# Kernel tuning notes

Hardware: AMD Instinct MI355X
Metric: run time of the kernel (lower is better)

Reference implementation:

```python
import jax, jax.numpy as jnp
import numpy as np

NUM_HEADS = 16
THETA = 10000.0


def apply_rope(x, pos, theta):
    # x: [B, H, S, d], pos: [S] int
    d = x.shape[-1]
    inv_freq = theta ** (-jnp.arange(0, d, 2, dtype=jnp.float32) / d)  # [d/2]
    ang = pos.astype(jnp.float32)[:, None] * inv_freq  # [S, d/2]
    cos, sin = jnp.cos(ang), jnp.sin(ang)
    x1, x2 = x[..., 0::2], x[..., 1::2]
    out_even = x1 * cos - x2 * sin
    out_odd = x1 * sin + x2 * cos
    return jnp.stack([out_even, out_odd], axis=-1).reshape(x.shape)


def setup_inputs() -> dict:
    key = jax.random.key(0)
    ks = jax.random.split(key, 5)
    B, S, D = 4, 2048, 2048
    s = 1.0 / np.sqrt(D)
    return {
        "x": jax.random.normal(ks[0], (B, S, D), dtype=jnp.float32),
        "token_positions": jnp.arange(S, dtype=jnp.int32),
        "wq": jax.random.normal(ks[1], (D, D), dtype=jnp.float32) * s,
        "wk": jax.random.normal(ks[2], (D, D), dtype=jnp.float32) * s,
        "wv": jax.random.normal(ks[3], (D, D), dtype=jnp.float32) * s,
        "wo": jax.random.normal(ks[4], (D, D), dtype=jnp.float32) * s,
    }


def reference(x, token_positions, wq, wk, wv, wo):
    B, S, _ = x.shape
    H = NUM_HEADS
    dh = wq.shape[0] // H

    def proj(w):
        y = jnp.einsum('bsd,ed->bse', x, w)  # Linear: x @ W^T
        return y.reshape(B, S, H, dh).transpose(0, 2, 1, 3)  # [B,H,S,dh]

    Q, K, V = proj(wq), proj(wk), proj(wv)
    Q = apply_rope(Q, token_positions, THETA)
    K = apply_rope(K, token_positions, THETA)

    scores = jnp.einsum('bhqd,bhkd->bhqk', Q, K) / jnp.sqrt(jnp.float32(dh))
    causal = jnp.tril(jnp.ones((S, S), dtype=bool))
    scores = jnp.where(causal, scores, jnp.finfo(scores.dtype).min)
    attn = jax.nn.softmax(scores, axis=-1)
    out = jnp.einsum('bhqk,bhkd->bhqd', attn, V)
    out = out.transpose(0, 2, 1, 3).reshape(B, S, H * dh)
    return jnp.einsum('bsd,ed->bse', out, wo)
```

## Files before the change

### kernel.cpp

```cpp
#include <hip/hip_runtime.h>
#include <math.h>

typedef __bf16 bf16;
typedef bf16 bf16x8 __attribute__((ext_vector_type(8)));
typedef bf16 bf16x4v __attribute__((ext_vector_type(4)));
typedef float f32x4 __attribute__((ext_vector_type(4)));

#define BB 4
#define SS 2048
#define DD 2048
#define HH 16
#define DH 128

__device__ __forceinline__ void gload_lds16(const bf16* g, bf16* l) {
  __builtin_amdgcn_global_load_lds(
      (const __attribute__((address_space(1))) void*)g,
      (__attribute__((address_space(3))) void*)l, 16, 0, 0);
}

__global__ __launch_bounds__(256) void cast_kernel(const float* __restrict__ in,
                                                   bf16* __restrict__ out, int n4) {
  int i = blockIdx.x * blockDim.x + threadIdx.x;
  if (i < n4) {
    const float4 v = ((const float4*)in)[i];
    bf16x4v o = {(bf16)v.x, (bf16)v.y, (bf16)v.z, (bf16)v.w};
    ((bf16x4v*)out)[i] = o;
  }
}

__global__ __launch_bounds__(256) void cast4_kernel(const float* __restrict__ w0,
                                                    const float* __restrict__ w1,
                                                    const float* __restrict__ w2,
                                                    const float* __restrict__ w3,
                                                    bf16* __restrict__ out) {
  const int i = blockIdx.x * blockDim.x + threadIdx.x;
  const int per = (DD * DD) / 4;
  const int sel = i / per, off = i - sel * per;
  const float* src = (sel == 0) ? w0 : (sel == 1) ? w1 : (sel == 2) ? w2 : w3;
  const float4 v = ((const float4*)src)[off];
  bf16x4v o = {(bf16)v.x, (bf16)v.y, (bf16)v.z, (bf16)v.w};
  ((bf16x4v*)(out + (size_t)sel * DD * DD))[off] = o;
}

template <int MODE>
__global__ __launch_bounds__(256) void gemm_bt(const bf16* __restrict__ A,
                                               const bf16* __restrict__ Bw,
                                               bf16* __restrict__ Cb,
                                               float* __restrict__ Cf,
                                               const int* __restrict__ pos,
                                               int M, int N, int K) {
  __shared__ alignas(16) bf16 lA[128 * 64];
  __shared__ alignas(16) bf16 lB[128 * 64];
  const int tid = threadIdx.x;
  const int wave = tid >> 6, lane = tid & 63;
  const int quad = lane >> 4, l15 = lane & 15;
  const int m0 = blockIdx.y * 128, n0 = blockIdx.x * 128;
  const int wm = (wave >> 1) * 64, wn = (wave & 1) * 64;

  f32x4 acc[4][4] = {};

  for (int k0 = 0; k0 < K; k0 += 64) {
    __syncthreads();
#pragma unroll
    for (int i = 0; i < 4; ++i) {
      const int p = (wave * 4 + i) * 64 + lane;
      const int r = p >> 3, c = p & 7;
      gload_lds16(A + (size_t)(m0 + r) * K + k0 + c * 8, lA + (size_t)(wave * 4 + i) * 512);
      gload_lds16(Bw + (size_t)(n0 + r) * K + k0 + c * 8, lB + (size_t)(wave * 4 + i) * 512);
    }
    __syncthreads();
#pragma unroll
    for (int kk = 0; kk < 2; ++kk) {
      bf16x8 af[4], bfr[4];
#pragma unroll
      for (int t = 0; t < 4; ++t)
        af[t] = *(const bf16x8*)(lA + (wm + t * 16 + l15) * 64 + kk * 32 + quad * 8);
#pragma unroll
      for (int t = 0; t < 4; ++t)
        bfr[t] = *(const bf16x8*)(lB + (wn + t * 16 + l15) * 64 + kk * 32 + quad * 8);
#pragma unroll
      for (int mt = 0; mt < 4; ++mt)
#pragma unroll
        for (int nt = 0; nt < 4; ++nt)
          acc[mt][nt] = __builtin_amdgcn_mfma_f32_16x16x32_bf16(af[mt], bfr[nt], acc[mt][nt], 0, 0, 0);
    }
  }

  float ps[4][4];
  if (MODE == 0) {
#pragma unroll
    for (int mt = 0; mt < 4; ++mt)
#pragma unroll
      for (int r = 0; r < 4; ++r)
        ps[mt][r] = (float)pos[(m0 + wm + mt * 16 + quad * 4 + r) & (SS - 1)];
  }

#pragma unroll
  for (int nt = 0; nt < 4; ++nt) {
    const int col = n0 + wn + nt * 16 + l15;
    float invf = 0.f, sgn = 0.f;
    if (MODE == 0) {
      const int d = col & (DH - 1);
      invf = exp2f((float)(d >> 1) * (-13.28771238f / 64.0f));
      sgn = (d & 1) ? 1.0f : -1.0f;
    }
#pragma unroll
    for (int mt = 0; mt < 4; ++mt) {
#pragma unroll
      for (int r = 0; r < 4; ++r) {
        const int row = m0 + wm + mt * 16 + quad * 4 + r;
        float v = acc[mt][nt][r];
        if (MODE == 0) {
          const float partner = __shfl_xor(v, 1);
          float sn, cn;
          __sincosf(ps[mt][r] * invf, &sn, &cn);
          v = fmaf(partner, sgn * sn, v * cn);
          const int b = row >> 11, s = row & (SS - 1);
          const int h = col >> 7, d = col & (DH - 1);
          Cb[((((size_t)b * HH + h) * SS + s) << 7) + d] = (bf16)v;
        } else if (MODE == 1) {
          const int b = row >> 11, s = row & (SS - 1);
          const int h = col >> 7, d = col & (DH - 1);
          Cb[(((size_t)b * HH + h) * DH + d) * SS + s] = (bf16)v;
        } else {
          Cf[(size_t)row * N + col] = v;
        }
      }
    }
  }
}

__global__ __launch_bounds__(256, 2) void flash_attn(const bf16* __restrict__ Q,
                                                     const bf16* __restrict__ Kg,
                                                     const bf16* __restrict__ Vt,
                                                     bf16* __restrict__ O) {
  __shared__ alignas(16) bf16 lK[2][64 * 128];
  __shared__ alignas(16) bf16 lV[2][128 * 64];
  __shared__ alignas(16) bf16 lP[4][16 * 64];

  const int tid = threadIdx.x;
  const int wave = tid >> 6, lane = tid & 63;
  const int quad = lane >> 4, l15 = lane & 15;
  const int swz = l15 & 7;
  const int bh = blockIdx.y;
  const int q0 = (gridDim.x - 1 - blockIdx.x) * 64;
  const bf16* Qh = Q + (size_t)bh * SS * DH;
  const bf16* Kh = Kg + (size_t)bh * SS * DH;
  const bf16* Vh = Vt + (size_t)bh * DH * SS;
  const int nkb = (q0 >> 6) + 1;

  bf16x8 qf[4];
#pragma unroll
  for (int t = 0; t < 4; ++t)
    qf[t] = *(const bf16x8*)(Qh + (size_t)(q0 + wave * 16 + l15) * DH + t * 32 + quad * 8);

  bf16* lPw = &lP[wave][0];
  const float cs = 0.12751649736f;
  const float MSTAT = 20.0f;
  float lsum = 0.f;
  f32x4 oacc[8] = {};

  auto stage = [&](bf16* kbuf, bf16* vbuf, int kb) {
#pragma unroll
    for (int j = 0; j < 4; ++j) {
      const int c = tid + j * 256;
      const int cb = wave * 64 + j * 256;
      const int kr = c >> 4;
      gload_lds16(Kh + (size_t)(kb * 64 + kr) * DH + (((c & 15) ^ (kr & 7)) * 8),
                  kbuf + (size_t)cb * 8);
      const int vr = c >> 3;
      gload_lds16(Vh + (size_t)vr * SS + kb * 64 + (((c & 7) ^ (vr & 7)) * 8),
                  vbuf + (size_t)cb * 8);
    }
  };

  int cur = 0;

  auto kv_iter = [&](bool diagf) {
    const bf16* kcur = lK[cur];
    const bf16* vcur = lV[cur];
    const int ktlim = diagf ? wave : 3;

    f32x4 sacc[4];
#pragma unroll
    for (int kt = 0; kt < 4; ++kt) sacc[kt] = (f32x4){0.f, 0.f, 0.f, 0.f};
    __builtin_amdgcn_s_setprio(1);
#pragma unroll
    for (int kt = 0; kt < 4; ++kt) {
      if (kt <= ktlim) {
#pragma unroll
        for (int t = 0; t < 4; ++t) {
          const bf16x8 kfrag =
              *(const bf16x8*)(kcur + (kt * 16 + l15) * 128 + (((t * 4 + quad) ^ swz) * 8));
          sacc[kt] = __builtin_amdgcn_mfma_f32_16x16x32_bf16(kfrag, qf[t], sacc[kt], 0, 0, 0);
        }
      }
    }
    __builtin_amdgcn_s_setprio(0);

#pragma unroll
    for (int kt = 0; kt < 4; ++kt) {
      bf16x4v pk = {(bf16)0.f, (bf16)0.f, (bf16)0.f, (bf16)0.f};
      if (kt <= ktlim) {
        float ls = 0.f;
#pragma unroll
        for (int r = 0; r < 4; ++r) {
          float e = exp2f(fmaf(sacc[kt][r], cs, -MSTAT));
          if (diagf && kt == wave && (quad * 4 + r) > l15) e = 0.f;
          ls += e;
          pk[r] = (bf16)e;
        }
        lsum += ls;
      }
      *(bf16x4v*)(lPw + l15 * 64 + (((kt * 2 + (quad >> 1)) ^ swz) * 8) + (quad & 1) * 4) = pk;
    }

    bf16x8 pa[2];
#pragma unroll
    for (int kc = 0; kc < 2; ++kc)
      pa[kc] = *(const bf16x8*)(lPw + l15 * 64 + (((kc * 4 + quad) ^ swz) * 8));

    __builtin_amdgcn_s_setprio(1);
#pragma unroll
    for (int db = 0; db < 8; ++db) {
#pragma unroll
      for (int kc = 0; kc < 2; ++kc) {
        const bf16x8 vfrag =
            *(const bf16x8*)(vcur + (db * 16 + l15) * 64 + (((kc * 4 + quad) ^ swz) * 8));
        oacc[db] = __builtin_amdgcn_mfma_f32_16x16x32_bf16(pa[kc], vfrag, oacc[db], 0, 0, 0);
      }
    }
    __builtin_amdgcn_s_setprio(0);
  };

  stage(lK[0], lV[0], 0);
  __syncthreads();

  for (int kb = 0; kb + 1 < nkb; ++kb) {
    stage(lK[cur ^ 1], lV[cur ^ 1], kb + 1);
    kv_iter(false);
    __syncthreads();
    cur ^= 1;
  }
  kv_iter(true);

  lsum += __shfl_xor(lsum, 16);
  lsum += __shfl_xor(lsum, 32);

  const int b = bh >> 4, h = bh & 15;
#pragma unroll
  for (int r = 0; r < 4; ++r) {
    const int q = quad * 4 + r;
    const float il = 1.0f / __shfl(lsum, q);
    bf16* orow = O + ((size_t)b * SS + q0 + wave * 16 + q) * DD + h * DH;
#pragma unroll
    for (int db = 0; db < 8; ++db) orow[db * 16 + l15] = (bf16)(oacc[db][r] * il);
  }
}

extern "C" void kernel_launch(void* const* d_in, const int* in_sizes, int n_in,
                              void* d_out, int out_size, void* d_ws, size_t ws_size,
                              hipStream_t stream) {
  (void)in_sizes; (void)n_in; (void)out_size; (void)ws_size;
  const float* x = (const float*)d_in[0];
  const int* pos = (const int*)d_in[1];
  const float* wq = (const float*)d_in[2];
  const float* wk = (const float*)d_in[3];
  const float* wv = (const float*)d_in[4];
  const float* wo = (const float*)d_in[5];
  float* out = (float*)d_out;

  bf16* xb  = (bf16*)d_ws;
  bf16* wqb = xb + (size_t)BB * SS * DD;
  bf16* wkb = wqb + (size_t)DD * DD;
  bf16* wvb = wkb + (size_t)DD * DD;
  bf16* wob = wvb + (size_t)DD * DD;
  bf16* Qb  = wob + (size_t)DD * DD;
  bf16* Kbf = Qb + (size_t)BB * SS * DD;
  bf16* Vtb = Kbf + (size_t)BB * SS * DD;
  bf16* Ob  = Vtb + (size_t)BB * SS * DD;

  const int nx = BB * SS * DD;
  cast_kernel<<<nx / 4 / 256, 256, 0, stream>>>(x, xb, nx / 4);
  cast4_kernel<<<DD * DD / 256, 256, 0, stream>>>(wq, wk, wv, wo, wqb);

  dim3 gg(DD / 128, (BB * SS) / 128);
  gemm_bt<0><<<gg, 256, 0, stream>>>(xb, wqb, Qb, nullptr, pos, BB * SS, DD, DD);
  gemm_bt<0><<<gg, 256, 0, stream>>>(xb, wkb, Kbf, nullptr, pos, BB * SS, DD, DD);
  gemm_bt<1><<<gg, 256, 0, stream>>>(xb, wvb, Vtb, nullptr, nullptr, BB * SS, DD, DD);

  flash_attn<<<dim3(SS / 64, BB * HH), 256, 0, stream>>>(Qb, Kbf, Vtb, Ob);

  gemm_bt<2><<<gg, 256, 0, stream>>>(Ob, wob, nullptr, out, nullptr, BB * SS, DD, DD);
}
```

Baseline: 775.1 us.

## Double query tile per block, read V straight from global, remap block order

```diff
diff --git a/kernel.cpp b/kernel.cpp
--- a/kernel.cpp
+++ b/kernel.cpp
@@ -135,55 +135,61 @@
                                                      const bf16* __restrict__ Vt,
                                                      bf16* __restrict__ O) {
   __shared__ alignas(16) bf16 lK[2][64 * 128];
-  __shared__ alignas(16) bf16 lV[2][128 * 64];
-  __shared__ alignas(16) bf16 lP[4][16 * 64];
+  __shared__ alignas(16) bf16 lP[4][32 * 64];
 
   const int tid = threadIdx.x;
   const int wave = tid >> 6, lane = tid & 63;
   const int quad = lane >> 4, l15 = lane & 15;
   const int swz = l15 & 7;
-  const int bh = blockIdx.y;
-  const int q0 = (gridDim.x - 1 - blockIdx.x) * 64;
+
+  const int lin = blockIdx.y * gridDim.x + blockIdx.x;
+  const int bh = ((lin & 7) << 3) | ((lin >> 3) & 7);
+  const int q0 = (15 - (lin >> 6)) * 128;
+
   const bf16* Qh = Q + (size_t)bh * SS * DH;
   const bf16* Kh = Kg + (size_t)bh * SS * DH;
   const bf16* Vh = Vt + (size_t)bh * DH * SS;
-  const int nkb = (q0 >> 6) + 1;
-
-  bf16x8 qf[4];
-#pragma unroll
-  for (int t = 0; t < 4; ++t)
-    qf[t] = *(const bf16x8*)(Qh + (size_t)(q0 + wave * 16 + l15) * DH + t * 32 + quad * 8);
+  const int nkb = (q0 >> 6) + 2;
+  const int qrow0 = q0 + wave * 32;
+
+  bf16x8 qf[2][4];
+#pragma unroll
+  for (int qt = 0; qt < 2; ++qt)
+#pragma unroll
+    for (int t = 0; t < 4; ++t)
+      qf[qt][t] = *(const bf16x8*)(Qh + (size_t)(qrow0 + qt * 16 + l15) * DH + t * 32 + quad * 8);
 
   bf16* lPw = &lP[wave][0];
   const float cs = 0.12751649736f;
   const float MSTAT = 20.0f;
-  float lsum = 0.f;
-  f32x4 oacc[8] = {};
-
-  auto stage = [&](bf16* kbuf, bf16* vbuf, int kb) {
+  float lsum[2] = {0.f, 0.f};
+  f32x4 oacc[2][8] = {};
+  int cur = 0;
+
+  auto stage = [&](int b, int kb) {
 #pragma unroll
     for (int j = 0; j < 4; ++j) {
       const int c = tid + j * 256;
-      const int cb = wave * 64 + j * 256;
       const int kr = c >> 4;
       gload_lds16(Kh + (size_t)(kb * 64 + kr) * DH + (((c & 15) ^ (kr & 7)) * 8),
-                  kbuf + (size_t)cb * 8);
-      const int vr = c >> 3;
-      gload_lds16(Vh + (size_t)vr * SS + kb * 64 + (((c & 7) ^ (vr & 7)) * 8),
-                  vbuf + (size_t)cb * 8);
+                  &lK[b][0] + (size_t)(wave * 64 + j * 256) * 8);
     }
   };
 
-  int cur = 0;
-
-  auto kv_iter = [&](bool diagf) {
-    const bf16* kcur = lK[cur];
-    const bf16* vcur = lV[cur];
-    const int ktlim = diagf ? wave : 3;
-
-    f32x4 sacc[4];
-#pragma unroll
-    for (int kt = 0; kt < 4; ++kt) sacc[kt] = (f32x4){0.f, 0.f, 0.f, 0.f};
+  auto kv_iter = [&](int kb, bool masked) {
+    int ktlim = 3;
+    if (masked) {
+      ktlim = (qrow0 + 31 - kb * 64) >> 4;
+      if (ktlim < 0) return;
+      if (ktlim > 3) ktlim = 3;
+    }
+    const bf16* kcur = &lK[cur][0];
+
+    f32x4 sacc[2][4];
+#pragma unroll
+    for (int qt = 0; qt < 2; ++qt)
+#pragma unroll
+      for (int kt = 0; kt < 4; ++kt) sacc[qt][kt] = (f32x4){0.f, 0.f, 0.f, 0.f};
     __builtin_amdgcn_s_setprio(1);
 #pragma unroll
     for (int kt = 0; kt < 4; ++kt) {
@@ -192,7 +198,8 @@
         for (int t = 0; t < 4; ++t) {
           const bf16x8 kfrag =
               *(const bf16x8*)(kcur + (kt * 16 + l15) * 128 + (((t * 4 + quad) ^ swz) * 8));
-          sacc[kt] = __builtin_amdgcn_mfma_f32_16x16x32_bf16(kfrag, qf[t], sacc[kt], 0, 0, 0);
+          sacc[0][kt] = __builtin_amdgcn_mfma_f32_16x16x32_bf16(kfrag, qf[0][t], sacc[0][kt], 0, 0, 0);
+          sacc[1][kt] = __builtin_amdgcn_mfma_f32_16x16x32_bf16(kfrag, qf[1][t], sacc[1][kt], 0, 0, 0);
         }
       }
     }
@@ -200,61 +207,86 @@
 
 #pragma unroll
     for (int kt = 0; kt < 4; ++kt) {
-      bf16x4v pk = {(bf16)0.f, (bf16)0.f, (bf16)0.f, (bf16)0.f};
-      if (kt <= ktlim) {
-        float ls = 0.f;
-#pragma unroll
-        for (int r = 0; r < 4; ++r) {
-          float e = exp2f(fmaf(sacc[kt][r], cs, -MSTAT));
-          if (diagf && kt == wave && (quad * 4 + r) > l15) e = 0.f;
-          ls += e;
-          pk[r] = (bf16)e;
+#pragma unroll
+      for (int qt = 0; qt < 2; ++qt) {
+        bf16x4v pk = {(bf16)0.f, (bf16)0.f, (bf16)0.f, (bf16)0.f};
+        if (kt <= ktlim) {
+          float ls = 0.f;
+#pragma unroll
+          for (int r = 0; r < 4; ++r) {
+            float e = exp2f(fmaf(sacc[qt][kt][r], cs, -MSTAT));
+            if (masked) {
+              const int key = kb * 64 + kt * 16 + quad * 4 + r;
+              if (key > qrow0 + qt * 16 + l15) e = 0.f;
+            }
+            ls += e;
+            pk[r] = (bf16)e;
+          }
+          lsum[qt] += ls;
         }
-        lsum += ls;
+        *(bf16x4v*)(lPw + (qt * 16 + l15) * 64 + (((kt * 2 + (quad >> 1)) ^ swz) * 8) +
+                    (quad & 1) * 4) = pk;
       }
-      *(bf16x4v*)(lPw + l15 * 64 + (((kt * 2 + (quad >> 1)) ^ swz) * 8) + (quad & 1) * 4) = pk;
-    }
-
-    bf16x8 pa[2];
-#pragma unroll
-    for (int kc = 0; kc < 2; ++kc)
-      pa[kc] = *(const bf16x8*)(lPw + l15 * 64 + (((kc * 4 + quad) ^ swz) * 8));
+    }
+
+    bf16x8 pa[2][2];
+#pragma unroll
+    for (int qt = 0; qt < 2; ++qt)
+#pragma unroll
+      for (int kc = 0; kc < 2; ++kc)
+        pa[qt][kc] = *(const bf16x8*)(lPw + (qt * 16 + l15) * 64 + (((kc * 4 + quad) ^ swz) * 8));
 
     __builtin_amdgcn_s_setprio(1);
 #pragma unroll
-    for (int db = 0; db < 8; ++db) {
-#pragma unroll
-      for (int kc = 0; kc < 2; ++kc) {
-        const bf16x8 vfrag =
-            *(const bf16x8*)(vcur + (db * 16 + l15) * 64 + (((kc * 4 + quad) ^ swz) * 8));
-        oacc[db] = __builtin_amdgcn_mfma_f32_16x16x32_bf16(pa[kc], vfrag, oacc[db], 0, 0, 0);
-      }
+    for (int g = 0; g < 2; ++g) {
+      bf16x8 vf[4][2];
+#pragma unroll
+      for (int d2 = 0; d2 < 4; ++d2)
+#pragma unroll
+        for (int kc = 0; kc < 2; ++kc)
+          vf[d2][kc] = *(const bf16x8*)(Vh + (size_t)((g * 4 + d2) * 16 + l15) * SS + kb * 64 +
+                                        kc * 32 + quad * 8);
+#pragma unroll
+      for (int d2 = 0; d2 < 4; ++d2)
+#pragma unroll
+        for (int kc = 0; kc < 2; ++kc) {
+          oacc[0][g * 4 + d2] =
+              __builtin_amdgcn_mfma_f32_16x16x32_bf16(pa[0][kc], vf[d2][kc], oacc[0][g * 4 + d2], 0, 0, 0);
+          oacc[1][g * 4 + d2] =
+              __builtin_amdgcn_mfma_f32_16x16x32_bf16(pa[1][kc], vf[d2][kc], oacc[1][g * 4 + d2], 0, 0, 0);
+        }
     }
     __builtin_amdgcn_s_setprio(0);
   };
 
-  stage(lK[0], lV[0], 0);
+  stage(0, 0);
   __syncthreads();
 
-  for (int kb = 0; kb + 1 < nkb; ++kb) {
-    stage(lK[cur ^ 1], lV[cur ^ 1], kb + 1);
-    kv_iter(false);
+  for (int kb = 0; kb < nkb - 1; ++kb) {
+    stage(cur ^ 1, kb + 1);
+    kv_iter(kb, kb + 2 >= nkb);
     __syncthreads();
     cur ^= 1;
   }
-  kv_iter(true);
-
-  lsum += __shfl_xor(lsum, 16);
-  lsum += __shfl_xor(lsum, 32);
+  kv_iter(nkb - 1, true);
+
+#pragma unroll
+  for (int qt = 0; qt < 2; ++qt) {
+    lsum[qt] += __shfl_xor(lsum[qt], 16);
+    lsum[qt] += __shfl_xor(lsum[qt], 32);
+  }
 
   const int b = bh >> 4, h = bh & 15;
 #pragma unroll
-  for (int r = 0; r < 4; ++r) {
-    const int q = quad * 4 + r;
-    const float il = 1.0f / __shfl(lsum, q);
-    bf16* orow = O + ((size_t)b * SS + q0 + wave * 16 + q) * DD + h * DH;
-#pragma unroll
-    for (int db = 0; db < 8; ++db) orow[db * 16 + l15] = (bf16)(oacc[db][r] * il);
+  for (int qt = 0; qt < 2; ++qt) {
+#pragma unroll
+    for (int r = 0; r < 4; ++r) {
+      const int qq = quad * 4 + r;
+      const float il = 1.0f / __shfl(lsum[qt], qq);
+      bf16* orow = O + ((size_t)b * SS + qrow0 + qt * 16 + qq) * DD + h * DH;
+#pragma unroll
+      for (int db = 0; db < 8; ++db) orow[db * 16 + l15] = (bf16)(oacc[qt][db][r] * il);
+    }
   }
 }
 
@@ -289,7 +321,7 @@
   gemm_bt<0><<<gg, 256, 0, stream>>>(xb, wkb, Kbf, nullptr, pos, BB * SS, DD, DD);
   gemm_bt<1><<<gg, 256, 0, stream>>>(xb, wvb, Vtb, nullptr, nullptr, BB * SS, DD, DD);
 
-  flash_attn<<<dim3(SS / 64, BB * HH), 256, 0, stream>>>(Qb, Kbf, Vtb, Ob);
+  flash_attn<<<dim3(SS / 128, BB * HH), 256, 0, stream>>>(Qb, Kbf, Vtb, Ob);
 
   gemm_bt<2><<<gg, 256, 0, stream>>>(Ob, wob, nullptr, out, nullptr, BB * SS, DD, DD);
 }
```

Result: faster. 730.3 us (-5.8%).
